# Performance work log

Measured on AMD Instinct MI355X. Metric: run time of the kernel, lower is better.

## Reference

```python
import jax, jax.numpy as jnp
import numpy as np

NUM_BINS = 256
SCALAR = 1.0


def _per_batch_hist(img):
    # img: [B, C, H, W] in [0,1]. torch.histc(img[i]*255, bins=256, min=0, max=255)
    # bin width = 255/256; value v maps to bin floor(v * 256/255), last edge -> bin 255.
    B = img.shape[0]
    x = img.reshape(B, -1) * 255.0
    idx = jnp.clip(jnp.floor(x * (NUM_BINS / 255.0)), 0, NUM_BINS - 1).astype(jnp.int32)
    # offset bin ids per batch item so one segment_sum builds all histograms
    seg = idx + (jnp.arange(B, dtype=jnp.int32)[:, None] * NUM_BINS)
    ones = jnp.ones_like(x)
    hist = jax.ops.segment_sum(ones.ravel(), seg.ravel(), num_segments=B * NUM_BINS)
    hist = hist.reshape(B, NUM_BINS)
    hist = hist / jnp.sum(hist, axis=1, keepdims=True)
    return hist.T  # [NUM_BINS, B] matching torch.stack(hist, dim=1)


def setup_inputs() -> dict:
    key = jax.random.key(0)
    k1, k2 = jax.random.split(key)
    im1 = jax.random.uniform(k1, (16, 3, 512, 512), dtype=jnp.float32)
    im2 = jax.random.uniform(k2, (16, 3, 512, 512), dtype=jnp.float32)
    return {"im1": im1, "im2": im2}


def reference(im1, im2):
    h1 = _per_batch_hist(im1)  # [256, B]
    h2 = _per_batch_hist(im2)
    c1 = jnp.cumsum(h1, axis=0)
    c2 = jnp.cumsum(h2, axis=0)
    emd = jnp.sum(jnp.abs(c1 - c2), axis=0)  # L1 over bin dim -> [B]
    total = jnp.sum(emd) / h2.shape[0] * SCALAR / 3.0
    return total
```

## Files before the change

### kernel.cpp

```cpp
#include <hip/hip_runtime.h>

#define NUM_BINS 256
#define PER_HIST 786432
#define BATCH 16
#define NHIST 32
#define CHUNKS 128
#define THREADS 256
#define ELEMS_PER_BLOCK (PER_HIST / CHUNKS)
#define VEC_PER_BLOCK (ELEMS_PER_BLOCK / 4)
#define ITERS (VEC_PER_BLOCK / THREADS)

typedef float floatx4 __attribute__((ext_vector_type(4)));

__global__ __launch_bounds__(THREADS) void hist_kernel(const float* __restrict__ im1,
                                                       const float* __restrict__ im2,
                                                       unsigned int* __restrict__ hist) {
    __shared__ unsigned int lh[4][4][NUM_BINS];
    const int t = threadIdx.x;
    const int w = t >> 6;
    const int sub = t & 3;

    #pragma unroll
    for (int i = 0; i < 4; ++i) {
        lh[i][0][t] = 0u; lh[i][1][t] = 0u; lh[i][2][t] = 0u; lh[i][3][t] = 0u;
    }
    __syncthreads();

    const int hid = blockIdx.y;
    const float* src = (hid < BATCH) ? im1 : im2;
    const int batch = hid & (BATCH - 1);
    const floatx4* p = (const floatx4*)(src + (size_t)batch * PER_HIST
                                            + (size_t)blockIdx.x * ELEMS_PER_BLOCK);

    floatx4 v[ITERS];
    #pragma unroll
    for (int i = 0; i < ITERS; ++i)
        v[i] = p[i * THREADS + t];

    const float scale = 256.0f;
    unsigned int* mh = lh[w][sub];

    #pragma unroll
    for (int i = 0; i < ITERS; ++i) {
        #pragma unroll
        for (int j = 0; j < 4; ++j) {
            int idx = (int)(v[i][j] * scale);
            atomicAdd(&mh[idx], 1u);
        }
    }
    __syncthreads();

    unsigned int sum = 0;
    #pragma unroll
    for (int i = 0; i < 4; ++i)
        sum += lh[i][0][t] + lh[i][1][t] + lh[i][2][t] + lh[i][3][t];
    atomicAdd(&hist[hid * NUM_BINS + t], sum);
}

__global__ __launch_bounds__(1024) void emd_kernel(const unsigned int* __restrict__ hist,
                                                   float* __restrict__ out) {
    __shared__ int batch_emd[BATCH];
    const int t = threadIdx.x;
    const int w = t >> 6;
    const int lane = t & 63;

    const uint4* h1 = (const uint4*)(hist + w * NUM_BINS);
    const uint4* h2 = (const uint4*)(hist + (BATCH + w) * NUM_BINS);
    uint4 a = h1[lane];
    uint4 b = h2[lane];

    int d0 = (int)(a.x - b.x);
    int d1 = (int)(a.y - b.y);
    int d2 = (int)(a.z - b.z);
    int d3 = (int)(a.w - b.w);

    int p0 = d0;
    int p1 = p0 + d1;
    int p2 = p1 + d2;
    int p3 = p2 + d3;

    int s = p3;
    #pragma unroll
    for (int off = 1; off < 64; off <<= 1) {
        int v = __shfl_up(s, off, 64);
        if (lane >= off) s += v;
    }
    int excl = s - p3;

    int c0 = excl + p0, c1 = excl + p1, c2 = excl + p2, c3 = excl + p3;
    int aa = (c0 < 0 ? -c0 : c0) + (c1 < 0 ? -c1 : c1)
           + (c2 < 0 ? -c2 : c2) + (c3 < 0 ? -c3 : c3);

    #pragma unroll
    for (int off = 32; off > 0; off >>= 1) aa += __shfl_xor(aa, off, 64);

    if (lane == 0) batch_emd[w] = aa;
    __syncthreads();

    if (t == 0) {
        long long acc = 0;
        #pragma unroll
        for (int i = 0; i < BATCH; ++i) acc += (long long)batch_emd[i];
        double total = (double)acc / (double)PER_HIST / (double)NUM_BINS / 3.0;
        out[0] = (float)total;
    }
}

extern "C" void kernel_launch(void* const* d_in, const int* in_sizes, int n_in,
                              void* d_out, int out_size, void* d_ws, size_t ws_size,
                              hipStream_t stream) {
    const float* im1 = (const float*)d_in[0];
    const float* im2 = (const float*)d_in[1];
    unsigned int* hist = (unsigned int*)d_ws;
    float* out = (float*)d_out;

    dim3 grid(CHUNKS, NHIST);
    hist_kernel<<<grid, THREADS, 0, stream>>>(im1, im2, hist);

    emd_kernel<<<1, 1024, 0, stream>>>(hist, out);
}
```

Measured before the change: 117.4 us.

## Use 32 bank-striped LDS histogram copies with software-pipelined loads and fewer blocks

Replaces the 16 per-wave/sub-lane histogram copies with 32 interleaved copies laid out so that each pair of lanes targets its own LDS bank. This is meant to cut bank conflicts and same-address atomic contention. Blocks per histogram drop from 128 to 32, so each thread handles 24 float4s, loaded in three batches of 8 that overlap the next load with the current atomics. The merge reads the copies with a rotated index to avoid conflicts and combines adjacent bins into one 64-bit global atomic, halving the global atomics. The cost is fewer blocks to fill the GPU (1024 total) and a 32KB LDS footprint, which may limit occupancy.

```diff
diff --git a/kernel.cpp b/kernel.cpp
--- a/kernel.cpp
+++ b/kernel.cpp
@@ -4,25 +4,28 @@
 #define PER_HIST 786432
 #define BATCH 16
 #define NHIST 32
-#define CHUNKS 128
+#define CHUNKS 32
 #define THREADS 256
 #define ELEMS_PER_BLOCK (PER_HIST / CHUNKS)
 #define VEC_PER_BLOCK (ELEMS_PER_BLOCK / 4)
-#define ITERS (VEC_PER_BLOCK / THREADS)
+#define VPT (VEC_PER_BLOCK / THREADS)
+#define VPB 8
+#define NCOPY 32
 
 typedef float floatx4 __attribute__((ext_vector_type(4)));
 
 __global__ __launch_bounds__(THREADS) void hist_kernel(const float* __restrict__ im1,
                                                        const float* __restrict__ im2,
                                                        unsigned int* __restrict__ hist) {
-    __shared__ unsigned int lh[4][4][NUM_BINS];
+    __shared__ unsigned int lh[NUM_BINS * NCOPY];
     const int t = threadIdx.x;
-    const int w = t >> 6;
-    const int sub = t & 3;
+    const unsigned int c = (unsigned int)((t & 63) >> 1);
 
-    #pragma unroll
-    for (int i = 0; i < 4; ++i) {
-        lh[i][0][t] = 0u; lh[i][1][t] = 0u; lh[i][2][t] = 0u; lh[i][3][t] = 0u;
+    {
+        uint4 z; z.x = z.y = z.z = z.w = 0u;
+        uint4* l4 = (uint4*)lh;
+        #pragma unroll
+        for (int j = 0; j < 8; ++j) l4[j * THREADS + t] = z;
     }
     __syncthreads();
 
@@ -32,29 +35,56 @@
     const floatx4* p = (const floatx4*)(src + (size_t)batch * PER_HIST
                                             + (size_t)blockIdx.x * ELEMS_PER_BLOCK);
 
-    floatx4 v[ITERS];
+    floatx4 va[VPB], vb[VPB];
     #pragma unroll
-    for (int i = 0; i < ITERS; ++i)
-        v[i] = p[i * THREADS + t];
+    for (int k = 0; k < VPB; ++k) va[k] = p[k * THREADS + t];
+    #pragma unroll
+    for (int k = 0; k < VPB; ++k) vb[k] = p[(VPB + k) * THREADS + t];
 
     const float scale = 256.0f;
-    unsigned int* mh = lh[w][sub];
 
     #pragma unroll
-    for (int i = 0; i < ITERS; ++i) {
+    for (int k = 0; k < VPB; ++k) {
         #pragma unroll
         for (int j = 0; j < 4; ++j) {
-            int idx = (int)(v[i][j] * scale);
-            atomicAdd(&mh[idx], 1u);
+            unsigned int idx = (unsigned int)(va[k][j] * scale);
+            atomicAdd(&lh[idx * NCOPY + c], 1u);
+        }
+    }
+    #pragma unroll
+    for (int k = 0; k < VPB; ++k) va[k] = p[(2 * VPB + k) * THREADS + t];
+    #pragma unroll
+    for (int k = 0; k < VPB; ++k) {
+        #pragma unroll
+        for (int j = 0; j < 4; ++j) {
+            unsigned int idx = (unsigned int)(vb[k][j] * scale);
+            atomicAdd(&lh[idx * NCOPY + c], 1u);
+        }
+    }
+    #pragma unroll
+    for (int k = 0; k < VPB; ++k) {
+        #pragma unroll
+        for (int j = 0; j < 4; ++j) {
+            unsigned int idx = (unsigned int)(va[k][j] * scale);
+            atomicAdd(&lh[idx * NCOPY + c], 1u);
         }
     }
     __syncthreads();
 
     unsigned int sum = 0;
+    const int r0 = t & 31;
     #pragma unroll
-    for (int i = 0; i < 4; ++i)
-        sum += lh[i][0][t] + lh[i][1][t] + lh[i][2][t] + lh[i][3][t];
-    atomicAdd(&hist[hid * NUM_BINS + t], sum);
+    for (int j = 0; j < NCOPY; ++j) {
+        int k = (j + r0) & 31;
+        sum += lh[t * NCOPY + k];
+    }
+
+    unsigned int other = __shfl_xor(sum, 1, 64);
+    if (!(t & 1)) {
+        unsigned long long s = (unsigned long long)sum
+                             | ((unsigned long long)other << 32);
+        atomicAdd((unsigned long long*)(hist + hid * NUM_BINS + t), s);
+    }
 }
 
 __global__ __launch_bounds__(1024) void emd_kernel(const unsigned int* __restrict__ hist,
```

New measurement: 117.7 us. About the same (+0.3%).
